# Performance work log

Measured on AMD Instinct MI355X. Metric: run time of the kernel, lower is better.

The kernel has to match this reference:

```python
import jax, jax.numpy as jnp
import numpy as np
from jax import lax

B, T, C = 4, 1024, 1024
H, HEAD = 16, 64            # n_head, head size (K == V == HEAD)
TM_DIM, TD_DIM = 32, 64     # TIME_MIX_EXTRA_DIM, W_MIX_EXTRA_DIM
N_LAYER, LAYER_ID = 24, 12
EPS = 1e-5
HEAD_DIV = 8.0              # head_size_divisor


def setup_inputs() -> dict:
    key = jax.random.key(0)
    ks = jax.random.split(key, 10)
    r1 = 1.0 - LAYER_ID / N_LAYER          # ratio_1_to_almost0
    r0 = LAYER_ID / max(N_LAYER - 1, 1)    # ratio_0_to_1
    ddd = np.arange(C, dtype=np.float64) / C
    x_maa = (1.0 - ddd ** r1).astype(np.float32)
    r_maa = (1.0 - ddd ** (0.5 * r1)).astype(np.float32)
    v_maa = (1.0 - (ddd ** r1 + 0.3 * r0)).astype(np.float32)
    n = np.arange(H * HEAD, dtype=np.float64)
    denom = max(H * HEAD - 1, 1)
    time_decay = (-6.0 + 5.0 * (n / denom) ** (0.7 + 1.3 * r0)).reshape(H, HEAD).astype(np.float32)
    zig = (((np.arange(H * HEAD) + 1) % 3) - 1) * 0.1
    time_first = (r0 * (1.0 - n / denom) + zig).reshape(H, HEAD).astype(np.float32)

    def unif(k, shape, s=0.01):
        return jax.random.uniform(k, shape, jnp.float32, -s, s)

    return {
        "x": jax.random.normal(ks[0], (B, T, C), jnp.float32),
        "x_maa": jnp.asarray(x_maa),
        "w_maa": jnp.asarray(x_maa),
        "k_maa": jnp.asarray(x_maa),
        "v_maa": jnp.asarray(v_maa),
        "r_maa": jnp.asarray(r_maa),
        "g_maa": jnp.asarray(r_maa),
        "tm_w1": unif(ks[1], (C, 5 * TM_DIM)),
        "tm_w2": unif(ks[2], (5, TM_DIM, C)),
        "td_w1": unif(ks[3], (C, TD_DIM)),
        "td_w2": unif(ks[4], (TD_DIM, C)),
        "time_decay": jnp.asarray(time_decay),
        "time_first": jnp.asarray(time_first),
        "Wr": jax.random.normal(ks[5], (C, H * HEAD), jnp.float32) * 0.02,
        "Wk": jax.random.normal(ks[6], (C, H * HEAD), jnp.float32) * 0.02,
        "Wv": jax.random.normal(ks[7], (C, H * HEAD), jnp.float32) * 0.02,
        "Wg": jax.random.normal(ks[8], (C, H * HEAD), jnp.float32) * 0.02,
        "Wo": jax.random.normal(ks[9], (H * HEAD, C), jnp.float32) * 0.02,
        "ln_w": jnp.ones((H * HEAD,), jnp.float32),
        "ln_b": jnp.zeros((H * HEAD,), jnp.float32),
    }


def reference(x, x_maa, w_maa, k_maa, v_maa, r_maa, g_maa,
              tm_w1, tm_w2, td_w1, td_w2, time_decay, time_first,
              Wr, Wk, Wv, Wg, Wo, ln_w, ln_b):
    B, T, C = x.shape
    H, K = time_decay.shape
    V = Wv.shape[1] // H
    # token shift: sx = x_{t-1} - x_t (zero-padded at t=0)
    sx = jnp.concatenate([jnp.zeros_like(x[:, :1]), x[:, :-1]], axis=1) - x
    # data-dependent token-mix LoRA: 5 mixing deltas
    mix = jnp.tanh((x + sx * x_maa) @ tm_w1).reshape(B, T, 5, TM_DIM)
    mix = jnp.einsum('btfd,fdc->fbtc', mix, tm_w2)  # [5,B,T,C]
    mw, mk, mv, mr, mg = mix
    wx = x + sx * (w_maa + mw)
    kx = x + sx * (k_maa + mk)
    vx = x + sx * (v_maa + mv)
    rx = x + sx * (r_maa + mr)
    gx = x + sx * (g_maa + mg)
    r = (rx @ Wr).reshape(B, T, H, K)
    k = (kx @ Wk).reshape(B, T, H, K)
    v = (vx @ Wv).reshape(B, T, H, V)
    g = jax.nn.silu(gx @ Wg)                         # [B,T,H*V]
    # data-dependent decay via LoRA, then double-exp squash into (0,1)
    w = time_decay[None, None] + (jnp.tanh(wx @ td_w1) @ td_w2).reshape(B, T, H, K)
    w = jnp.exp(-jnp.exp(w))                         # [B,T,H,K]
    u = time_first                                   # [H,K]

    def step(s, inp):
        rt, kt, vt, wt = inp                         # [B,H,K],[B,H,K],[B,H,V],[B,H,K]
        kv = kt[..., None] * vt[..., None, :]        # [B,H,K,V] outer product
        y = jnp.einsum('bhk,bhkv->bhv', rt, s + u[None, :, :, None] * kv)
        return wt[..., None] * s + kv, y

    s0 = jnp.zeros((B, H, K, V), x.dtype)
    xs = (jnp.moveaxis(r, 1, 0), jnp.moveaxis(k, 1, 0),
          jnp.moveaxis(v, 1, 0), jnp.moveaxis(w, 1, 0))
    _, ys = lax.scan(step, s0, xs)                   # ys: [T,B,H,V]
    out = jnp.moveaxis(ys, 0, 1).reshape(B, T, H, V) / HEAD_DIV
    # GroupNorm with n_kv_head groups over dim_v channels -> per-head norm
    mu = out.mean(-1, keepdims=True)
    var = out.var(-1, keepdims=True)
    out = ((out - mu) * lax.rsqrt(var + EPS)).reshape(B, T, H * V) * ln_w + ln_b
    return (out * g) @ Wo
```

## Files before the change

### kernel.cpp

```cpp
#include <hip/hip_runtime.h>
#include <hip/hip_bf16.h>
#include <math.h>
#include <stdint.h>

constexpr int Bn = 4, Tn = 1024, Cn = 1024, Hn = 16;
constexpr int BT = Bn * Tn;
constexpr long long BTC = (long long)BT * Cn;
constexpr int CL = 64;
constexpr int NC = Tn / CL;

typedef __bf16 bf16x8_t __attribute__((ext_vector_type(8)));
typedef float f32x4_t __attribute__((ext_vector_type(4)));
typedef unsigned short us8_t __attribute__((ext_vector_type(8)));

__device__ __forceinline__ unsigned short f2bf_bits(float v) {
    __hip_bfloat16 h = __float2bfloat16(v);
    return *reinterpret_cast<unsigned short*>(&h);
}
__device__ __forceinline__ float bfbits2f(unsigned short u) {
    unsigned int x = (unsigned int)u << 16;
    return __uint_as_float(x);
}

__device__ __forceinline__ void gload16(const void* g, void* l) {
    auto const* gp = reinterpret_cast<const unsigned int __attribute__((address_space(1)))*>(
        reinterpret_cast<uintptr_t>(g));
    auto* lp = reinterpret_cast<unsigned int __attribute__((address_space(3)))*>(
        reinterpret_cast<uintptr_t>(l));
    __builtin_amdgcn_global_load_lds(gp, lp, 16, 0, 0);
}

__global__ __launch_bounds__(256) void prep_mixin(const float* __restrict__ x,
                                                  const float* __restrict__ x_maa,
                                                  __hip_bfloat16* __restrict__ out) {
    long long q = (long long)blockIdx.x * 256 + threadIdx.x;
    if (q * 4 >= BTC) return;
    long long idx = q * 4;
    int c = (int)(idx & (Cn - 1));
    long long bt = idx >> 10;
    int t = (int)(bt & (Tn - 1));
    float4 xv = *reinterpret_cast<const float4*>(x + idx);
    float4 xp = (t > 0) ? *reinterpret_cast<const float4*>(x + idx - Cn)
                        : make_float4(0.f, 0.f, 0.f, 0.f);
    float4 ma = *reinterpret_cast<const float4*>(x_maa + c);
    ushort4 o;
    o.x = f2bf_bits(xv.x + (xp.x - xv.x) * ma.x);
    o.y = f2bf_bits(xv.y + (xp.y - xv.y) * ma.y);
    o.z = f2bf_bits(xv.z + (xp.z - xv.z) * ma.z);
    o.w = f2bf_bits(xv.w + (xp.w - xv.w) * ma.w);
    *reinterpret_cast<ushort4*>(out + idx) = o;
}

__global__ __launch_bounds__(256) void transp5(const float* __restrict__ W0,
                                               const float* __restrict__ W1,
                                               const float* __restrict__ W2,
                                               const float* __restrict__ W3,
                                               const float* __restrict__ W4,
                                               __hip_bfloat16* __restrict__ T0,
                                               __hip_bfloat16* __restrict__ T1,
                                               __hip_bfloat16* __restrict__ T2,
                                               __hip_bfloat16* __restrict__ T3,
                                               __hip_bfloat16* __restrict__ T4) {
    int z = blockIdx.z;
    const float* W = (z == 0) ? W0 : (z == 1) ? W1 : (z == 2) ? W2 : (z == 3) ? W3 : W4;
    __hip_bfloat16* Wt = (z == 0) ? T0 : (z == 1) ? T1 : (z == 2) ? T2 : (z == 3) ? T3 : T4;
    __shared__ float tile[32][33];
    int c0 = blockIdx.x * 32, r0 = blockIdx.y * 32;
    int tx = threadIdx.x & 31, ty = threadIdx.x >> 5;
    #pragma unroll
    for (int i = 0; i < 4; i++)
        tile[ty + 8 * i][tx] = W[(size_t)(r0 + ty + 8 * i) * Cn + c0 + tx];
    __syncthreads();
    #pragma unroll
    for (int i = 0; i < 4; i++)
        Wt[(size_t)(c0 + ty + 8 * i) * Cn + r0 + tx] = __float2bfloat16(tile[tx][ty + 8 * i]);
}

__global__ __launch_bounds__(256) void transp_bf16(const float* __restrict__ W,
                                                   __hip_bfloat16* __restrict__ Wt,
                                                   int R, int Cc) {
    __shared__ float tile[32][33];
    int c0 = blockIdx.x * 32, r0 = blockIdx.y * 32;
    int tx = threadIdx.x & 31, ty = threadIdx.x >> 5;
    #pragma unroll
    for (int i = 0; i < 4; i++)
        tile[ty + 8 * i][tx] = W[(size_t)(r0 + ty + 8 * i) * Cc + c0 + tx];
    __syncthreads();
    #pragma unroll
    for (int i = 0; i < 4; i++)
        Wt[(size_t)(c0 + ty + 8 * i) * R + r0 + tx] = __float2bfloat16(tile[tx][ty + 8 * i]);
}

template <int EPI>
__global__ __launch_bounds__(256) void gemm_f32(const float* __restrict__ A,
                                                const float* __restrict__ Bm,
                                                float* __restrict__ C,
                                                int M, int N, int K,
                                                const float* __restrict__ extra) {
    __shared__ float As[16][64];
    __shared__ float Bs[16][64];
    int tid = threadIdx.x;
    int m0 = blockIdx.y * 64, n0 = blockIdx.x * 64;
    int tx = tid & 15, ty = tid >> 4;
    int ar = tid >> 2, ac = (tid & 3) * 4;
    int br = tid >> 4, bc = (tid & 15) * 4;
    float acc[4][4] = {};

    for (int k0 = 0; k0 < K; k0 += 16) {
        const float* ap = A + (size_t)(m0 + ar) * K + k0 + ac;
        float4 av = *reinterpret_cast<const float4*>(ap);
        As[ac + 0][ar] = av.x; As[ac + 1][ar] = av.y;
        As[ac + 2][ar] = av.z; As[ac + 3][ar] = av.w;
        float4 bv = *reinterpret_cast<const float4*>(Bm + (size_t)(k0 + br) * N + n0 + bc);
        *reinterpret_cast<float4*>(&Bs[br][bc]) = bv;
        __syncthreads();
        #pragma unroll
        for (int kk = 0; kk < 16; kk++) {
            float4 a4 = *reinterpret_cast<const float4*>(&As[kk][ty * 4]);
            float4 b4 = *reinterpret_cast<const float4*>(&Bs[kk][tx * 4]);
            float aa[4] = {a4.x, a4.y, a4.z, a4.w};
            float bb[4] = {b4.x, b4.y, b4.z, b4.w};
            #pragma unroll
            for (int i = 0; i < 4; i++)
                #pragma unroll
                for (int j = 0; j < 4; j++)
                    acc[i][j] = fmaf(aa[i], bb[j], acc[i][j]);
        }
        __syncthreads();
    }

    #pragma unroll
    for (int i = 0; i < 4; i++) {
        int row = m0 + ty * 4 + i;
        #pragma unroll
        for (int j = 0; j < 4; j++) {
            int col = n0 + tx * 4 + j;
            float v = acc[i][j];
            if (EPI == 3) v = -expf(extra[col] + v);
            C[(size_t)row * N + col] = v;
        }
    }
}

template <int KS>
__global__ __launch_bounds__(256) void gemm_f32_splitk(const float* __restrict__ A,
                                                       const float* __restrict__ Bm,
                                                       float* __restrict__ part,
                                                       int M, int N, int K) {
    __shared__ float As[16][64];
    __shared__ float Bs[16][64];
    int tid = threadIdx.x;
    int kp = blockIdx.x;
    int m0 = blockIdx.y * 64;
    int kbeg = kp * (K / KS), kend = kbeg + K / KS;
    int tx = tid & 15, ty = tid >> 4;
    int ar = tid >> 2, ac = (tid & 3) * 4;
    int br = tid >> 4, bc = (tid & 15) * 4;
    float acc[4][4] = {};

    for (int k0 = kbeg; k0 < kend; k0 += 16) {
        float4 av = *reinterpret_cast<const float4*>(A + (size_t)(m0 + ar) * K + k0 + ac);
        As[ac + 0][ar] = av.x; As[ac + 1][ar] = av.y;
        As[ac + 2][ar] = av.z; As[ac + 3][ar] = av.w;
        *reinterpret_cast<float4*>(&Bs[br][bc]) =
            *reinterpret_cast<const float4*>(Bm + (size_t)(k0 + br) * N + bc);
        __syncthreads();
        #pragma unroll
        for (int kk = 0; kk < 16; kk++) {
            float4 a4 = *reinterpret_cast<const float4*>(&As[kk][ty * 4]);
            float4 b4 = *reinterpret_cast<const float4*>(&Bs[kk][tx * 4]);
            float aa[4] = {a4.x, a4.y, a4.z, a4.w};
            float bb[4] = {b4.x, b4.y, b4.z, b4.w};
            #pragma unroll
            for (int i = 0; i < 4; i++)
                #pragma unroll
                for (int j = 0; j < 4; j++)
                    acc[i][j] = fmaf(aa[i], bb[j], acc[i][j]);
        }
        __syncthreads();
    }
    #pragma unroll
    for (int i = 0; i < 4; i++) {
        int row = m0 + ty * 4 + i;
        #pragma unroll
        for (int j = 0; j < 4; j++)
            part[((size_t)kp * M + row) * N + tx * 4 + j] = acc[i][j];
    }
}

template <int KS>
__global__ __launch_bounds__(256) void splitk_reduce_tanh(const float* __restrict__ part,
                                                          float* __restrict__ outp,
                                                          int total, size_t stride) {
    int i = blockIdx.x * 256 + threadIdx.x;
    if (i >= total) return;
    float s = 0.f;
    #pragma unroll
    for (int kp = 0; kp < KS; kp++) s += part[kp * stride + i];
    outp[i] = tanhf(s);
}

template <int KS>
__global__ __launch_bounds__(256) void gemm_mfma_sk(const __hip_bfloat16* __restrict__ A,
                                                    const __hip_bfloat16* __restrict__ Bt,
                                                    float* __restrict__ part,
                                                    int M, int N, int K) {
    __shared__ alignas(16) unsigned short As[64 * 64];
    __shared__ alignas(16) unsigned short Bs[128 * 64];
    int tid = threadIdx.x;
    int m0 = blockIdx.y * 64, n0 = blockIdx.x * 128;
    int kp = blockIdx.z;
    int kbeg = kp * (K / KS), kend = kbeg + K / KS;
    int wave = tid >> 6, lane = tid & 63;
    int wm = (wave & 1) * 32, wn = (wave >> 1) * 64;
    int l15 = lane & 15, l4 = lane >> 4;
    f32x4_t acc[2][4] = {};

    for (int k0 = kbeg; k0 < kend; k0 += 64) {
        #pragma unroll
        for (int p = 0; p < 2; p++) {
            int cch = tid + p * 256;
            int row = cch >> 3, slot = cch & 7;
            int s2 = slot ^ (row & 7);
            *reinterpret_cast<us8_t*>(&As[row * 64 + s2 * 8]) =
                *reinterpret_cast<const us8_t*>(&A[(size_t)(m0 + row) * K + k0 + slot * 8]);
        }
        #pragma unroll
        for (int p = 0; p < 4; p++) {
            int cch = tid + p * 256;
            int row = cch >> 3, slot = cch & 7;
            int s2 = slot ^ (row & 7);
            int rowg = n0 + row; if (rowg > N - 1) rowg = N - 1;
            *reinterpret_cast<us8_t*>(&Bs[row * 64 + s2 * 8]) =
                *reinterpret_cast<const us8_t*>(&Bt[(size_t)rowg * K + k0 + slot * 8]);
        }
        __syncthreads();
        #pragma unroll
        for (int kw = 0; kw < 2; kw++) {
            int slot = kw * 4 + l4;
            bf16x8_t af[2], bfr[4];
            #pragma unroll
            for (int f = 0; f < 2; f++) {
                int ar = wm + f * 16 + l15;
                af[f] = *reinterpret_cast<const bf16x8_t*>(&As[ar * 64 + (slot ^ (ar & 7)) * 8]);
            }
            #pragma unroll
            for (int f = 0; f < 4; f++) {
                int br = wn + f * 16 + l15;
                bfr[f] = *reinterpret_cast<const bf16x8_t*>(&Bs[br * 64 + (slot ^ (br & 7)) * 8]);
            }
            #pragma unroll
            for (int i = 0; i < 2; i++)
                #pragma unroll
                for (int j = 0; j < 4; j++)
                    acc[i][j] = __builtin_amdgcn_mfma_f32_16x16x32_bf16(af[i], bfr[j], acc[i][j], 0, 0, 0);
        }
        __syncthreads();
    }

    #pragma unroll
    for (int i = 0; i < 2; i++) {
        int rbase = m0 + wm + i * 16 + l4 * 4;
        #pragma unroll
        for (int j = 0; j < 4; j++) {
            int col = n0 + wn + j * 16 + l15;
            if (col < N) {
                #pragma unroll
                for (int q = 0; q < 4; q++)
                    part[((size_t)kp * M + rbase + q) * N + col] = acc[i][j][q];
            }
        }
    }
}

__global__ __launch_bounds__(256) void gemm_qkvg(const __hip_bfloat16* __restrict__ A0,
                                                 const __hip_bfloat16* __restrict__ A1,
                                                 const __hip_bfloat16* __restrict__ A2,
                                                 const __hip_bfloat16* __restrict__ A3,
                                                 const __hip_bfloat16* __restrict__ B0,
                                                 const __hip_bfloat16* __restrict__ B1,
                                                 const __hip_bfloat16* __restrict__ B2,
                                                 const __hip_bfloat16* __restrict__ B3,
                                                 __hip_bfloat16* __restrict__ C0,
                                                 __hip_bfloat16* __restrict__ C1,
                                                 __hip_bfloat16* __restrict__ C2,
                                                 __hip_bfloat16* __restrict__ C3,
                                                 int M, int N, int K) {
    int g = blockIdx.z;
    const __hip_bfloat16* A  = (g == 0) ? A0 : (g == 1) ? A1 : (g == 2) ? A2 : A3;
    const __hip_bfloat16* Bt = (g == 0) ? B0 : (g == 1) ? B1 : (g == 2) ? B2 : B3;
    __hip_bfloat16* Co = (g == 0) ? C0 : (g == 1) ? C1 : (g == 2) ? C2 : C3;
    __shared__ alignas(16) unsigned short As[64 * 64];
    __shared__ alignas(16) unsigned short Bs[128 * 64];
    int tid = threadIdx.x;
    int m0 = blockIdx.x * 64, n0 = blockIdx.y * 128;
    int wave = tid >> 6, lane = tid & 63;
    int wm = (wave & 1) * 32, wn = (wave >> 1) * 64;
    int l15 = lane & 15, l4 = lane >> 4;
    int lrow = lane >> 3, ls2 = lane & 7;
    f32x4_t acc[2][4] = {};

    for (int k0 = 0; k0 < K; k0 += 64) {
        #pragma unroll
        for (int ci = 0; ci < 2; ci++) {
            int r0 = wave * 16 + ci * 8;
            int row = r0 + lrow;
            int gs = ls2 ^ (row & 7);
            gload16(&A[(size_t)(m0 + row) * K + k0 + gs * 8], &As[r0 * 64]);
        }
        #pragma unroll
        for (int ci = 0; ci < 4; ci++) {
            int r0 = wave * 32 + ci * 8;
            int row = r0 + lrow;
            int gs = ls2 ^ (row & 7);
            gload16(&Bt[(size_t)(n0 + row) * K + k0 + gs * 8], &Bs[r0 * 64]);
        }
        __syncthreads();
        #pragma unroll
        for (int kw = 0; kw < 2; kw++) {
            int slot = kw * 4 + l4;
            bf16x8_t af[2], bfr[4];
            #pragma unroll
            for (int f = 0; f < 2; f++) {
                int ar = wm + f * 16 + l15;
                af[f] = *reinterpret_cast<const bf16x8_t*>(&As[ar * 64 + (slot ^ (ar & 7)) * 8]);
            }
            #pragma unroll
            for (int f = 0; f < 4; f++) {
                int br = wn + f * 16 + l15;
                bfr[f] = *reinterpret_cast<const bf16x8_t*>(&Bs[br * 64 + (slot ^ (br & 7)) * 8]);
            }
            #pragma unroll
            for (int i = 0; i < 2; i++)
                #pragma unroll
                for (int j = 0; j < 4; j++)
                    acc[i][j] = __builtin_amdgcn_mfma_f32_16x16x32_bf16(af[i], bfr[j], acc[i][j], 0, 0, 0);
        }
        __syncthreads();
    }

    #pragma unroll
    for (int i = 0; i < 2; i++) {
        int rbase = m0 + wm + i * 16 + l4 * 4;
        #pragma unroll
        for (int j = 0; j < 4; j++) {
            int col = n0 + wn + j * 16 + l15;
            #pragma unroll
            for (int q = 0; q < 4; q++) {
                float v = acc[i][j][q];
                if (g == 3) v = v / (1.f + expf(-v));
                Co[(size_t)(rbase + q) * N + col] = __float2bfloat16(v);
            }
        }
    }
}

__global__ __launch_bounds__(256) void gemm_mfma_gl(const __hip_bfloat16* __restrict__ A,
                                                    const __hip_bfloat16* __restrict__ Bt,
                                                    float* __restrict__ Cout,
                                                    int M, int N, int K) {
    __shared__ alignas(16) unsigned short As[64 * 64];
    __shared__ alignas(16) unsigned short Bs[128 * 64];
    int tid = threadIdx.x;
    int m0 = blockIdx.x * 64, n0 = blockIdx.y * 128;
    int wave = tid >> 6, lane = tid & 63;
    int wm = (wave & 1) * 32, wn = (wave >> 1) * 64;
    int l15 = lane & 15, l4 = lane >> 4;
    int lrow = lane >> 3, ls2 = lane & 7;
    f32x4_t acc[2][4] = {};

    for (int k0 = 0; k0 < K; k0 += 64) {
        #pragma unroll
        for (int ci = 0; ci < 2; ci++) {
            int r0 = wave * 16 + ci * 8;
            int row = r0 + lrow;
            int gs = ls2 ^ (row & 7);
            gload16(&A[(size_t)(m0 + row) * K + k0 + gs * 8], &As[r0 * 64]);
        }
        #pragma unroll
        for (int ci = 0; ci < 4; ci++) {
            int r0 = wave * 32 + ci * 8;
            int row = r0 + lrow;
            int gs = ls2 ^ (row & 7);
            gload16(&Bt[(size_t)(n0 + row) * K + k0 + gs * 8], &Bs[r0 * 64]);
        }
        __syncthreads();
        #pragma unroll
        for (int kw = 0; kw < 2; kw++) {
            int slot = kw * 4 + l4;
            bf16x8_t af[2], bfr[4];
            #pragma unroll
            for (int f = 0; f < 2; f++) {
                int ar = wm + f * 16 + l15;
                af[f] = *reinterpret_cast<const bf16x8_t*>(&As[ar * 64 + (slot ^ (ar & 7)) * 8]);
            }
            #pragma unroll
            for (int f = 0; f < 4; f++) {
                int br = wn + f * 16 + l15;
                bfr[f] = *reinterpret_cast<const bf16x8_t*>(&Bs[br * 64 + (slot ^ (br & 7)) * 8]);
            }
            #pragma unroll
            for (int i = 0; i < 2; i++)
                #pragma unroll
                for (int j = 0; j < 4; j++)
                    acc[i][j] = __builtin_amdgcn_mfma_f32_16x16x32_bf16(af[i], bfr[j], acc[i][j], 0, 0, 0);
        }
        __syncthreads();
    }

    #pragma unroll
    for (int i = 0; i < 2; i++) {
        int rbase = m0 + wm + i * 16 + l4 * 4;
        #pragma unroll
        for (int j = 0; j < 4; j++) {
            int col = n0 + wn + j * 16 + l15;
            #pragma unroll
            for (int q = 0; q < 4; q++)
                Cout[(size_t)(rbase + q) * N + col] = acc[i][j][q];
        }
    }
}

__global__ __launch_bounds__(256) void deltas_mix(const float* __restrict__ x,
                                                  const float* __restrict__ mix160,
                                                  const float* __restrict__ w2,
                                                  const float* __restrict__ wmaa,
                                                  const float* __restrict__ kmaa,
                                                  const float* __restrict__ vmaa,
                                                  const float* __restrict__ rmaa,
                                                  const float* __restrict__ gmaa,
                                                  float* __restrict__ wx,
                                                  __hip_bfloat16* __restrict__ kxb,
                                                  __hip_bfloat16* __restrict__ vxb,
                                                  __hip_bfloat16* __restrict__ rxb,
                                                  __hip_bfloat16* __restrict__ gxb) {
    int tid = threadIdx.x;
    int c4 = tid * 4;
    int r0 = blockIdx.x * 4;
    const float* mrow = mix160 + (size_t)r0 * 160;
    float xv[4][4], sx[4][4];
    #pragma unroll
    for (int r = 0; r < 4; r++) {
        int row = r0 + r;
        int t = row & (Tn - 1);
        size_t idx = (size_t)row * Cn + c4;
        float4 xvv = *reinterpret_cast<const float4*>(x + idx);
        float4 xp = (t > 0) ? *reinterpret_cast<const float4*>(x + idx - Cn)
                            : make_float4(0.f, 0.f, 0.f, 0.f);
        xv[r][0] = xvv.x; xv[r][1] = xvv.y; xv[r][2] = xvv.z; xv[r][3] = xvv.w;
        sx[r][0] = xp.x - xvv.x; sx[r][1] = xp.y - xvv.y;
        sx[r][2] = xp.z - xvv.z; sx[r][3] = xp.w - xvv.w;
    }
    #pragma unroll
    for (int f = 0; f < 5; f++) {
        float acc[4][4] = {};
        for (int dd = 0; dd < 32; dd++) {
            float4 wv = *reinterpret_cast<const float4*>(w2 + (size_t)(f * 32 + dd) * Cn + c4);
            float wvv[4] = {wv.x, wv.y, wv.z, wv.w};
            #pragma unroll
            for (int r = 0; r < 4; r++) {
                float ms = mrow[r * 160 + f * 32 + dd];
                #pragma unroll
                for (int j = 0; j < 4; j++)
                    acc[r][j] = fmaf(ms, wvv[j], acc[r][j]);
            }
        }
        const float* maa = (f == 0) ? wmaa : (f == 1) ? kmaa : (f == 2) ? vmaa
                         : (f == 3) ? rmaa : gmaa;
        float4 mv4 = *reinterpret_cast<const float4*>(maa + c4);
        float mvv[4] = {mv4.x, mv4.y, mv4.z, mv4.w};
        #pragma unroll
        for (int r = 0; r < 4; r++) {
            size_t idx = (size_t)(r0 + r) * Cn + c4;
            float val[4];
            #pragma unroll
            for (int j = 0; j < 4; j++)
                val[j] = xv[r][j] + sx[r][j] * (mvv[j] + acc[r][j]);
            if (f == 0) {
                *reinterpret_cast<float4*>(wx + idx) =
                    make_float4(val[0], val[1], val[2], val[3]);
            } else {
                ushort4 o;
                o.x = f2bf_bits(val[0]); o.y = f2bf_bits(val[1]);
                o.z = f2bf_bits(val[2]); o.w = f2bf_bits(val[3]);
                __hip_bfloat16* dst = (f == 1) ? kxb : (f == 2) ? vxb : (f == 3) ? rxb : gxb;
                *reinterpret_cast<ushort4*>(dst + idx) = o;
            }
        }
    }
}

__global__ __launch_bounds__(256) void chunk_summary(const __hip_bfloat16* __restrict__ kb,
                                                     const __hip_bfloat16* __restrict__ vb,
                                                     const float* __restrict__ lw,
                                                     float* __restrict__ Bc,
                                                     float* __restrict__ Wtot) {
    int bid = blockIdx.x;
    int c = bid & 15, h = (bid >> 4) & 15, b = bid >> 8;
    size_t gbase = ((size_t)(b * Tn + c * CL) * Hn + h) * 64;
    int tid = threadIdx.x;
    __shared__ float linc[64][68];
    __shared__ float wtp[4][64];
    __shared__ alignas(16) __hip_bfloat16 kdT[64][72];
    __shared__ alignas(16) __hip_bfloat16 vsT[64][72];
    int wave = tid >> 6, lane = tid & 63;
    {
        float acc = 0.f;
        #pragma unroll
        for (int i = 0; i < 16; i++) {
            int t = wave * 16 + i;
            acc += lw[gbase + (size_t)t * 1024 + lane];
            linc[t][lane] = acc;
        }
        wtp[wave][lane] = acc;
    }
    __syncthreads();
    {
        float off = 0.f;
        for (int g = 0; g < wave; g++) off += wtp[g][lane];
        #pragma unroll
        for (int i = 0; i < 16; i++) linc[wave * 16 + i][lane] += off;
    }
    __syncthreads();
    int t4 = tid >> 2, c0 = (tid & 3) * 16;
    #pragma unroll
    for (int i = 0; i < 4; i++) {
        int ch = c0 + i * 4;
        size_t ga = gbase + (size_t)t4 * 1024 + ch;
        ushort4 ku = *reinterpret_cast<const ushort4*>(kb + ga);
        ushort4 vu = *reinterpret_cast<const ushort4*>(vb + ga);
        float kk[4] = {bfbits2f(ku.x), bfbits2f(ku.y), bfbits2f(ku.z), bfbits2f(ku.w)};
        float vv[4] = {bfbits2f(vu.x), bfbits2f(vu.y), bfbits2f(vu.z), bfbits2f(vu.w)};
        #pragma unroll
        for (int j = 0; j < 4; j++) {
            float li = linc[t4][ch + j];
            float lend = linc[63][ch + j];
            kdT[ch + j][t4] = __float2bfloat16(kk[j] * expf(lend - li));
            vsT[ch + j][t4] = __float2bfloat16(vv[j]);
        }
    }
    if (tid < 64) Wtot[(size_t)bid * 64 + tid] = expf(linc[63][tid]);
    __syncthreads();
    int l15 = lane & 15, l4q = lane >> 4;
    #pragma unroll
    for (int nt = 0; nt < 4; nt++) {
        f32x4_t acc = {};
        #pragma unroll
        for (int kt = 0; kt < 2; kt++) {
            bf16x8_t a = *reinterpret_cast<const bf16x8_t*>(&kdT[wave * 16 + l15][kt * 32 + l4q * 8]);
            bf16x8_t bb = *reinterpret_cast<const bf16x8_t*>(&vsT[nt * 16 + l15][kt * 32 + l4q * 8]);
            acc = __builtin_amdgcn_mfma_f32_16x16x32_bf16(a, bb, acc, 0, 0, 0);
        }
        #pragma unroll
        for (int q = 0; q < 4; q++) {
            int krow = wave * 16 + l4q * 4 + q;
            Bc[(size_t)bid * 4096 + (size_t)krow * 64 + nt * 16 + l15] = acc[q];
        }
    }
}

__global__ __launch_bounds__(256) void chunk_scan(const float* __restrict__ Bc,
                                                  const float* __restrict__ Wtot,
                                                  float* __restrict__ SbufT) {
    int bid = blockIdx.x;
    int bh = bid >> 2, vg = bid & 3;
    int kk = threadIdx.x >> 2;
    int v = vg * 16 + (threadIdx.x & 3) * 4;
    float4 S = make_float4(0.f, 0.f, 0.f, 0.f);
    for (int c = 0; c < NC; c++) {
        size_t base = (size_t)(bh * NC + c) * 4096;
        SbufT[base + (size_t)(v + 0) * 64 + kk] = S.x;
        SbufT[base + (size_t)(v + 1) * 64 + kk] = S.y;
        SbufT[base + (size_t)(v + 2) * 64 + kk] = S.z;
        SbufT[base + (size_t)(v + 3) * 64 + kk] = S.w;
        float wt = Wtot[(size_t)(bh * NC + c) * 64 + kk];
        float4 b4 = *reinterpret_cast<const float4*>(Bc + base + (size_t)kk * 64 + v);
        S.x = fmaf(wt, S.x, b4.x);
        S.y = fmaf(wt, S.y, b4.y);
        S.z = fmaf(wt, S.z, b4.z);
        S.w = fmaf(wt, S.w, b4.w);
    }
}

__global__ __launch_bounds__(256) void chunk_out(const __hip_bfloat16* __restrict__ rb,
                                                 const __hip_bfloat16* __restrict__ kb,
                                                 const __hip_bfloat16* __restrict__ vb,
                                                 const float* __restrict__ lw,
                                                 const float* __restrict__ SbufT,
                                                 const float* __restrict__ tf,
                                                 float* __restrict__ y) {
    int bid = blockIdx.x;
    int c = bid & 15, h = (bid >> 4) & 15, b = bid >> 8;
    size_t gbase = ((size_t)(b * Tn + c * CL) * Hn + h) * 64;
    int tid = threadIdx.x;
    __shared__ alignas(16) __hip_bfloat16 qs[64][72];
    __shared__ alignas(16) __hip_bfloat16 ks[64][72];
    __shared__ alignas(16) __hip_bfloat16 vsT[64][72];
    __shared__ alignas(16) __hip_bfloat16 scT[64][72];
    __shared__ alignas(16) float uni[64 * 68];
    __shared__ float wtp[4][64];
    __shared__ float diag[64];
    float (*linc)[68] = reinterpret_cast<float(*)[68]>(uni);
    __hip_bfloat16 (*asb)[72] = reinterpret_cast<__hip_bfloat16(*)[72]>(uni);
    int wave = tid >> 6, lane = tid & 63;
    {
        float acc = 0.f;
        #pragma unroll
        for (int i = 0; i < 16; i++) {
            int t = wave * 16 + i;
            acc += lw[gbase + (size_t)t * 1024 + lane];
            linc[t][lane] = acc;
        }
        wtp[wave][lane] = acc;
    }
    __syncthreads();
    {
        float off = 0.f;
        for (int g = 0; g < wave; g++) off += wtp[g][lane];
        #pragma unroll
        for (int i = 0; i < 16; i++) linc[wave * 16 + i][lane] += off;
    }
    __syncthreads();
    int t4 = tid >> 2, c0 = (tid & 3) * 16;
    float dpart = 0.f;
    #pragma unroll
    for (int i = 0; i < 4; i++) {
        int ch = c0 + i * 4;
        size_t ga = gbase + (size_t)t4 * 1024 + ch;
        ushort4 ru = *reinterpret_cast<const ushort4*>(rb + ga);
        ushort4 ku = *reinterpret_cast<const ushort4*>(kb + ga);
        ushort4 vu = *reinterpret_cast<const ushort4*>(vb + ga);
        float4 l4v = *reinterpret_cast<const float4*>(lw + ga);
        float4 u4 = *reinterpret_cast<const float4*>(tf + h * 64 + ch);
        float4 s4 = *reinterpret_cast<const float4*>(SbufT + (size_t)bid * 4096 + (size_t)t4 * 64 + ch);
        float rr[4] = {bfbits2f(ru.x), bfbits2f(ru.y), bfbits2f(ru.z), bfbits2f(ru.w)};
        float kkv[4] = {bfbits2f(ku.x), bfbits2f(ku.y), bfbits2f(ku.z), bfbits2f(ku.w)};
        float vv[4] = {bfbits2f(vu.x), bfbits2f(vu.y), bfbits2f(vu.z), bfbits2f(vu.w)};
        float lwv[4] = {l4v.x, l4v.y, l4v.z, l4v.w};
        float uu[4] = {u4.x, u4.y, u4.z, u4.w};
        float ss[4] = {s4.x, s4.y, s4.z, s4.w};
        #pragma unroll
        for (int j = 0; j < 4; j++) {
            float li = linc[t4][ch + j];
            qs[t4][ch + j] = __float2bfloat16(rr[j] * expf(li - lwv[j]));
            ks[t4][ch + j] = __float2bfloat16(kkv[j] * expf(-li));
            vsT[ch + j][t4] = __float2bfloat16(vv[j]);
            scT[t4][ch + j] = __float2bfloat16(ss[j]);
            dpart = fmaf(rr[j] * uu[j], kkv[j], dpart);
        }
    }
    dpart += __shfl_xor(dpart, 1);
    dpart += __shfl_xor(dpart, 2);
    if ((tid & 3) == 0) diag[t4] = dpart;
    __syncthreads();
    int l15 = lane & 15, l4q = lane >> 4;
    #pragma unroll
    for (int nt = 0; nt < 4; nt++) {
        f32x4_t acc = {};
        if (nt <= wave) {
            #pragma unroll
            for (int kt = 0; kt < 2; kt++) {
                bf16x8_t a = *reinterpret_cast<const bf16x8_t*>(&qs[wave * 16 + l15][kt * 32 + l4q * 8]);
                bf16x8_t bb = *reinterpret_cast<const bf16x8_t*>(&ks[nt * 16 + l15][kt * 32 + l4q * 8]);
                acc = __builtin_amdgcn_mfma_f32_16x16x32_bf16(a, bb, acc, 0, 0, 0);
            }
        }
        #pragma unroll
        for (int q = 0; q < 4; q++) {
            int t = wave * 16 + l4q * 4 + q;
            int tau = nt * 16 + l15;
            float v = (tau < t) ? acc[q] : (tau == t ? diag[t] : 0.f);
            asb[t][tau] = __float2bfloat16(v);
        }
    }
    __syncthreads();
    #pragma unroll
    for (int nt = 0; nt < 4; nt++) {
        f32x4_t acc = {};
        int kmax = (wave >> 1) + 1;
        for (int kt = 0; kt < kmax; kt++) {
            bf16x8_t a = *reinterpret_cast<const bf16x8_t*>(&asb[wave * 16 + l15][kt * 32 + l4q * 8]);
            bf16x8_t bb = *reinterpret_cast<const bf16x8_t*>(&vsT[nt * 16 + l15][kt * 32 + l4q * 8]);
            acc = __builtin_amdgcn_mfma_f32_16x16x32_bf16(a, bb, acc, 0, 0, 0);
        }
        #pragma unroll
        for (int kt = 0; kt < 2; kt++) {
            bf16x8_t a = *reinterpret_cast<const bf16x8_t*>(&qs[wave * 16 + l15][kt * 32 + l4q * 8]);
            bf16x8_t bb = *reinterpret_cast<const bf16x8_t*>(&scT[nt * 16 + l15][kt * 32 + l4q * 8]);
            acc = __builtin_amdgcn_mfma_f32_16x16x32_bf16(a, bb, acc, 0, 0, 0);
        }
        #pragma unroll
        for (int q = 0; q < 4; q++) {
            int t = wave * 16 + l4q * 4 + q;
            y[gbase + (size_t)t * 1024 + nt * 16 + l15] = acc[q];
        }
    }
}

__global__ __launch_bounds__(256) void gn_mul(const float* __restrict__ y,
                                              const __hip_bfloat16* __restrict__ g,
                                              const float* __restrict__ lnw,
                                              const float* __restrict__ lnb,
                                              __hip_bfloat16* __restrict__ fin) {
    int tid = threadIdx.x;
    int lane = tid & 63;
    int wv = tid >> 6;
    int grp = blockIdx.x * 4 + wv;
    int h = grp & 15;
    size_t idx = (size_t)grp * 64 + lane;
    float val = y[idx] * 0.125f;
    float sum = val, sq = val * val;
    #pragma unroll
    for (int off = 32; off > 0; off >>= 1) {
        sum += __shfl_xor(sum, off, 64);
        sq  += __shfl_xor(sq,  off, 64);
    }
    float mu = sum * (1.f / 64.f);
    float var = sq * (1.f / 64.f) - mu * mu;
    float rs = rsqrtf(var + 1e-5f);
    float o = (val - mu) * rs * lnw[h * 64 + lane] + lnb[h * 64 + lane];
    fin[idx] = __float2bfloat16(o * __bfloat162float(g[idx]));
}

extern "C" void kernel_launch(void* const* d_in, const int* in_sizes, int n_in,
                              void* d_out, int out_size, void* d_ws, size_t ws_size,
                              hipStream_t stream) {
    (void)in_sizes; (void)n_in; (void)out_size; (void)ws_size;
    const float* x      = (const float*)d_in[0];
    const float* x_maa  = (const float*)d_in[1];
    const float* w_maa  = (const float*)d_in[2];
    const float* k_maa  = (const float*)d_in[3];
    const float* v_maa  = (const float*)d_in[4];
    const float* r_maa  = (const float*)d_in[5];
    const float* g_maa  = (const float*)d_in[6];
    const float* tm_w1  = (const float*)d_in[7];
    const float* tm_w2  = (const float*)d_in[8];
    const float* td_w1  = (const float*)d_in[9];
    const float* td_w2  = (const float*)d_in[10];
    const float* t_dec  = (const float*)d_in[11];
    const float* t_first= (const float*)d_in[12];
    const float* Wr     = (const float*)d_in[13];
    const float* Wk     = (const float*)d_in[14];
    const float* Wv     = (const float*)d_in[15];
    const float* Wg     = (const float*)d_in[16];
    const float* Wo     = (const float*)d_in[17];
    const float* ln_w   = (const float*)d_in[18];
    const float* ln_b   = (const float*)d_in[19];
    float* out = (float*)d_out;

    char* ws = (char*)d_ws;
    size_t off = 0;
    auto alloc = [&](size_t bytes) -> void* {
        void* p = ws + off;
        off = (off + bytes + 255) & ~(size_t)255;
        return p;
    };
    __hip_bfloat16* mixin = (__hip_bfloat16*)alloc(BTC * 2);
    float* mix160 = (float*)alloc((size_t)BT * 160 * 4);
    float* wxr    = (float*)alloc(BTC * 4);
    __hip_bfloat16* kxb = (__hip_bfloat16*)alloc(BTC * 2);
    __hip_bfloat16* vxb = (__hip_bfloat16*)alloc(BTC * 2);
    __hip_bfloat16* rxb = (__hip_bfloat16*)alloc(BTC * 2);
    __hip_bfloat16* gxb = (__hip_bfloat16*)alloc(BTC * 2);
    __hip_bfloat16* kb  = (__hip_bfloat16*)alloc(BTC * 2);
    __hip_bfloat16* vb  = (__hip_bfloat16*)alloc(BTC * 2);
    __hip_bfloat16* gb  = (__hip_bfloat16*)alloc(BTC * 2);
    float* wl1 = (float*)alloc((size_t)BT * 64 * 4);
    float* lwb = (float*)alloc(BTC * 4);
    __hip_bfloat16* WrT = (__hip_bfloat16*)alloc((size_t)Cn * Cn * 2);
    __hip_bfloat16* WkT = (__hip_bfloat16*)alloc((size_t)Cn * Cn * 2);
    __hip_bfloat16* WvT = (__hip_bfloat16*)alloc((size_t)Cn * Cn * 2);
    __hip_bfloat16* WgT = (__hip_bfloat16*)alloc((size_t)Cn * Cn * 2);
    __hip_bfloat16* WoT = (__hip_bfloat16*)alloc((size_t)Cn * Cn * 2);
    __hip_bfloat16* tmw1T = (__hip_bfloat16*)alloc((size_t)160 * Cn * 2);
    float* skpart = (float*)alloc((size_t)8 * BT * 64 * 4);
    float* lorapart = (float*)alloc((size_t)4 * BT * 160 * 4);
    __hip_bfloat16* rb = mixin;
    float* BcB   = wxr;
    float* ybuf  = wxr;
    float* WtB   = wl1;
    float* SbufT = (float*)rxb;
    __hip_bfloat16* fin = kxb;

    dim3 blk(256);
    transp5<<<dim3(32, 32, 5), blk, 0, stream>>>(Wr, Wk, Wv, Wg, Wo,
                                                 WrT, WkT, WvT, WgT, WoT);
    transp_bf16<<<dim3(5, 32), blk, 0, stream>>>(tm_w1, tmw1T, Cn, 160);
    prep_mixin<<<dim3((unsigned)(BTC / 1024)), blk, 0, stream>>>(x, x_maa, mixin);
    gemm_mfma_sk<4><<<dim3(2, 64, 4), blk, 0, stream>>>(mixin, tmw1T, lorapart, BT, 160, Cn);
    splitk_reduce_tanh<4><<<dim3((BT * 160 + 255) / 256), blk, 0, stream>>>(
        lorapart, mix160, BT * 160, (size_t)BT * 160);
    deltas_mix<<<dim3(BT / 4), blk, 0, stream>>>(x, mix160, tm_w2,
                                                 w_maa, k_maa, v_maa, r_maa, g_maa,
                                                 wxr, kxb, vxb, rxb, gxb);
    gemm_qkvg<<<dim3(64, 8, 4), blk, 0, stream>>>(rxb, kxb, vxb, gxb,
                                                  WrT, WkT, WvT, WgT,
                                                  rb, kb, vb, gb, BT, Cn, Cn);
    gemm_f32_splitk<8><<<dim3(8, 64), blk, 0, stream>>>(wxr, td_w1, skpart, BT, 64, Cn);
    splitk_reduce_tanh<8><<<dim3(BT * 64 / 256), blk, 0, stream>>>(skpart, wl1, BT * 64,
                                                                   (size_t)BT * 64);
    gemm_f32<3><<<dim3(16, 64), blk, 0, stream>>>(wl1, td_w2, lwb, BT, Cn, 64, t_dec);
    chunk_summary<<<dim3(Bn * Hn * NC), blk, 0, stream>>>(kb, vb, lwb, BcB, WtB);
    chunk_scan<<<dim3(Bn * Hn * 4), blk, 0, stream>>>(BcB, WtB, SbufT);
    chunk_out<<<dim3(Bn * Hn * NC), blk, 0, stream>>>(rb, kb, vb, lwb, SbufT, t_first, ybuf);
    gn_mul<<<dim3(BT * Hn / 4), blk, 0, stream>>>(ybuf, gb, ln_w, ln_b, fin);
    gemm_mfma_gl<<<dim3(64, 8), blk, 0, stream>>>(fin, WoT, out, BT, Cn, Cn);
}
```

Measured before the change: 216.0 us.

## Replace scalar FP32 LoRA-delta mix with bf16 MFMA GEMM plus elementwise fuse kernel

Replaces the FP32 FMA-loop deltas_mix kernel with two kernels. The first is a bf16 MFMA GEMM (K=32 per mix factor) that writes five delta tensors in bf16. The second is an elementwise kernel that combines x, the shifted x, the maa vectors and the deltas into the mixed inputs. The tanh'd LoRA activations and tm_w2 are now stored in bf16, and the workspace is shared between lorapart, skpart and the deltas. This moves the small matmul onto tensor cores at the cost of an extra 5xBTC bf16 round trip through memory and reduced precision in the deltas.

```diff
diff --git a/kernel.cpp b/kernel.cpp
--- a/kernel.cpp
+++ b/kernel.cpp
@@ -201,6 +201,18 @@
 }
 
 template <int KS>
+__global__ __launch_bounds__(256) void splitk_reduce_tanh_bf(const float* __restrict__ part,
+                                                             __hip_bfloat16* __restrict__ outp,
+                                                             int total, size_t stride) {
+    int i = blockIdx.x * 256 + threadIdx.x;
+    if (i >= total) return;
+    float s = 0.f;
+    #pragma unroll
+    for (int kp = 0; kp < KS; kp++) s += part[kp * stride + i];
+    outp[i] = __float2bfloat16(tanhf(s));
+}
+
+template <int KS>
 __global__ __launch_bounds__(256) void gemm_mfma_sk(const __hip_bfloat16* __restrict__ A,
                                                     const __hip_bfloat16* __restrict__ Bt,
                                                     float* __restrict__ part,
@@ -269,6 +281,109 @@
                 for (int q = 0; q < 4; q++)
                     part[((size_t)kp * M + rbase + q) * N + col] = acc[i][j][q];
             }
+        }
+    }
+}
+
+__global__ __launch_bounds__(256) void dmix_gemm(const __hip_bfloat16* __restrict__ A,
+                                                 const __hip_bfloat16* __restrict__ W2T,
+                                                 __hip_bfloat16* __restrict__ D) {
+    __shared__ alignas(16) unsigned short As[64 * 32];
+    __shared__ alignas(16) unsigned short Bs[128 * 32];
+    int tid = threadIdx.x;
+    int m0 = blockIdx.x * 64, n0 = blockIdx.y * 128;
+    int f  = blockIdx.z;
+    int wave = tid >> 6, lane = tid & 63;
+    int wm = (wave & 1) * 32, wn = (wave >> 1) * 64;
+    int l15 = lane & 15, l4 = lane >> 4;
+    int lrow2 = lane >> 2, ls = lane & 3;
+    f32x4_t acc[2][4] = {};
+
+    {
+        int row = wave * 16 + lrow2;
+        int gs = ls ^ (row & 3);
+        gload16(&A[(size_t)(m0 + row) * 160 + f * 32 + gs * 8], &As[(wave * 16) * 32]);
+    }
+    #pragma unroll
+    for (int ci = 0; ci < 2; ci++) {
+        int r0 = wave * 32 + ci * 16;
+        int row = r0 + lrow2;
+        int gs = ls ^ (row & 3);
+        gload16(&W2T[(size_t)(n0 + row) * 160 + f * 32 + gs * 8], &Bs[r0 * 32]);
+    }
+    __syncthreads();
+    bf16x8_t af[2], bfr[4];
+    #pragma unroll
+    for (int i = 0; i < 2; i++) {
+        int ar = wm + i * 16 + l15;
+        af[i] = *reinterpret_cast<const bf16x8_t*>(&As[ar * 32 + ((l4 ^ (ar & 3)) * 8)]);
+    }
+    #pragma unroll
+    for (int j = 0; j < 4; j++) {
+        int br = wn + j * 16 + l15;
+        bfr[j] = *reinterpret_cast<const bf16x8_t*>(&Bs[br * 32 + ((l4 ^ (br & 3)) * 8)]);
+    }
+    #pragma unroll
+    for (int i = 0; i < 2; i++)
+        #pragma unroll
+        for (int j = 0; j < 4; j++)
+            acc[i][j] = __builtin_amdgcn_mfma_f32_16x16x32_bf16(af[i], bfr[j], acc[i][j], 0, 0, 0);
+
+    __hip_bfloat16* Df = D + (size_t)f * BTC;
+    #pragma unroll
+    for (int i = 0; i < 2; i++) {
+        int rbase = m0 + wm + i * 16 + l4 * 4;
+        #pragma unroll
+        for (int j = 0; j < 4; j++) {
+            int col = n0 + wn + j * 16 + l15;
+            #pragma unroll
+            for (int q = 0; q < 4; q++)
+                Df[(size_t)(rbase + q) * Cn + col] = __float2bfloat16(acc[i][j][q]);
+        }
+    }
+}
+
+__global__ __launch_bounds__(256) void dmix_fuse(const float* __restrict__ x,
+                                                 const __hip_bfloat16* __restrict__ D,
+                                                 const float* __restrict__ wmaa,
+                                                 const float* __restrict__ kmaa,
+                                                 const float* __restrict__ vmaa,
+                                                 const float* __restrict__ rmaa,
+                                                 const float* __restrict__ gmaa,
+                                                 float* __restrict__ wx,
+                                                 __hip_bfloat16* __restrict__ kxb,
+                                                 __hip_bfloat16* __restrict__ vxb,
+                                                 __hip_bfloat16* __restrict__ rxb,
+                                                 __hip_bfloat16* __restrict__ gxb) {
+    long long q = (long long)blockIdx.x * 256 + threadIdx.x;
+    if (q * 4 >= BTC) return;
+    long long idx = q * 4;
+    int c = (int)(idx & (Cn - 1));
+    int t = (int)((idx >> 10) & (Tn - 1));
+    float4 xv = *reinterpret_cast<const float4*>(x + idx);
+    float4 xp = (t > 0) ? *reinterpret_cast<const float4*>(x + idx - Cn)
+                        : make_float4(0.f, 0.f, 0.f, 0.f);
+    float sx[4] = {xp.x - xv.x, xp.y - xv.y, xp.z - xv.z, xp.w - xv.w};
+    float xvv[4] = {xv.x, xv.y, xv.z, xv.w};
+    #pragma unroll
+    for (int f = 0; f < 5; f++) {
+        const float* maa = (f == 0) ? wmaa : (f == 1) ? kmaa : (f == 2) ? vmaa
+                         : (f == 3) ? rmaa : gmaa;
+        float4 m4 = *reinterpret_cast<const float4*>(maa + c);
+        float mm[4] = {m4.x, m4.y, m4.z, m4.w};
+        ushort4 d4 = *reinterpret_cast<const ushort4*>(D + (size_t)f * BTC + idx);
+        float dd[4] = {bfbits2f(d4.x), bfbits2f(d4.y), bfbits2f(d4.z), bfbits2f(d4.w)};
+        float val[4];
+        #pragma unroll
+        for (int j = 0; j < 4; j++) val[j] = xvv[j] + sx[j] * (mm[j] + dd[j]);
+        if (f == 0) {
+            *reinterpret_cast<float4*>(wx + idx) = make_float4(val[0], val[1], val[2], val[3]);
+        } else {
+            ushort4 o;
+            o.x = f2bf_bits(val[0]); o.y = f2bf_bits(val[1]);
+            o.z = f2bf_bits(val[2]); o.w = f2bf_bits(val[3]);
+            __hip_bfloat16* dst = (f == 1) ? kxb : (f == 2) ? vxb : (f == 3) ? rxb : gxb;
+            *reinterpret_cast<ushort4*>(dst + idx) = o;
         }
     }
 }
@@ -421,75 +536,6 @@
     }
 }
 
-__global__ __launch_bounds__(256) void deltas_mix(const float* __restrict__ x,
-                                                  const float* __restrict__ mix160,
-                                                  const float* __restrict__ w2,
-                                                  const float* __restrict__ wmaa,
-                                                  const float* __restrict__ kmaa,
-                                                  const float* __restrict__ vmaa,
-                                                  const float* __restrict__ rmaa,
-                                                  const float* __restrict__ gmaa,
-                                                  float* __restrict__ wx,
-                                                  __hip_bfloat16* __restrict__ kxb,
-                                                  __hip_bfloat16* __restrict__ vxb,
-                                                  __hip_bfloat16* __restrict__ rxb,
-                                                  __hip_bfloat16* __restrict__ gxb) {
-    int tid = threadIdx.x;
-    int c4 = tid * 4;
-    int r0 = blockIdx.x * 4;
-    const float* mrow = mix160 + (size_t)r0 * 160;
-    float xv[4][4], sx[4][4];
-    #pragma unroll
-    for (int r = 0; r < 4; r++) {
-        int row = r0 + r;
-        int t = row & (Tn - 1);
-        size_t idx = (size_t)row * Cn + c4;
-        float4 xvv = *reinterpret_cast<const float4*>(x + idx);
-        float4 xp = (t > 0) ? *reinterpret_cast<const float4*>(x + idx - Cn)
-                            : make_float4(0.f, 0.f, 0.f, 0.f);
-        xv[r][0] = xvv.x; xv[r][1] = xvv.y; xv[r][2] = xvv.z; xv[r][3] = xvv.w;
-        sx[r][0] = xp.x - xvv.x; sx[r][1] = xp.y - xvv.y;
-        sx[r][2] = xp.z - xvv.z; sx[r][3] = xp.w - xvv.w;
-    }
-    #pragma unroll
-    for (int f = 0; f < 5; f++) {
-        float acc[4][4] = {};
-        for (int dd = 0; dd < 32; dd++) {
-            float4 wv = *reinterpret_cast<const float4*>(w2 + (size_t)(f * 32 + dd) * Cn + c4);
-            float wvv[4] = {wv.x, wv.y, wv.z, wv.w};
-            #pragma unroll
-            for (int r = 0; r < 4; r++) {
-                float ms = mrow[r * 160 + f * 32 + dd];
-                #pragma unroll
-                for (int j = 0; j < 4; j++)
-                    acc[r][j] = fmaf(ms, wvv[j], acc[r][j]);
-            }
-        }
-        const float* maa = (f == 0) ? wmaa : (f == 1) ? kmaa : (f == 2) ? vmaa
-                         : (f == 3) ? rmaa : gmaa;
-        float4 mv4 = *reinterpret_cast<const float4*>(maa + c4);
-        float mvv[4] = {mv4.x, mv4.y, mv4.z, mv4.w};
-        #pragma unroll
-        for (int r = 0; r < 4; r++) {
-            size_t idx = (size_t)(r0 + r) * Cn + c4;
-            float val[4];
-            #pragma unroll
-            for (int j = 0; j < 4; j++)
-                val[j] = xv[r][j] + sx[r][j] * (mvv[j] + acc[r][j]);
-            if (f == 0) {
-                *reinterpret_cast<float4*>(wx + idx) =
-                    make_float4(val[0], val[1], val[2], val[3]);
-            } else {
-                ushort4 o;
-                o.x = f2bf_bits(val[0]); o.y = f2bf_bits(val[1]);
-                o.z = f2bf_bits(val[2]); o.w = f2bf_bits(val[3]);
-                __hip_bfloat16* dst = (f == 1) ? kxb : (f == 2) ? vxb : (f == 3) ? rxb : gxb;
-                *reinterpret_cast<ushort4*>(dst + idx) = o;
-            }
-        }
-    }
-}
-
 __global__ __launch_bounds__(256) void chunk_summary(const __hip_bfloat16* __restrict__ kb,
                                                      const __hip_bfloat16* __restrict__ vb,
                                                      const float* __restrict__ lw,
@@ -756,7 +802,7 @@
         return p;
     };
     __hip_bfloat16* mixin = (__hip_bfloat16*)alloc(BTC * 2);
-    float* mix160 = (float*)alloc((size_t)BT * 160 * 4);
+    __hip_bfloat16* mix160b = (__hip_bfloat16*)alloc((size_t)BT * 160 * 2);
     float* wxr    = (float*)alloc(BTC * 4);
     __hip_bfloat16* kxb = (__hip_bfloat16*)alloc(BTC * 2);
     __hip_bfloat16* vxb = (__hip_bfloat16*)alloc(BTC * 2);
@@ -773,8 +819,11 @@
     __hip_bfloat16* WgT = (__hip_bfloat16*)alloc((size_t)Cn * Cn * 2);
     __hip_bfloat16* WoT = (__hip_bfloat16*)alloc((size_t)Cn * Cn * 2);
     __hip_bfloat16* tmw1T = (__hip_bfloat16*)alloc((size_t)160 * Cn * 2);
-    float* skpart = (float*)alloc((size_t)8 * BT * 64 * 4);
-    float* lorapart = (float*)alloc((size_t)4 * BT * 160 * 4);
+    __hip_bfloat16* w2T   = (__hip_bfloat16*)alloc((size_t)Cn * 160 * 2);
+    char* big = (char*)alloc((size_t)5 * BTC * 2);
+    float* lorapart = (float*)big;
+    __hip_bfloat16* d5 = (__hip_bfloat16*)big;
+    float* skpart = (float*)big;
     __hip_bfloat16* rb = mixin;
     float* BcB   = wxr;
     float* ybuf  = wxr;
@@ -786,13 +835,15 @@
     transp5<<<dim3(32, 32, 5), blk, 0, stream>>>(Wr, Wk, Wv, Wg, Wo,
                                                  WrT, WkT, WvT, WgT, WoT);
     transp_bf16<<<dim3(5, 32), blk, 0, stream>>>(tm_w1, tmw1T, Cn, 160);
+    transp_bf16<<<dim3(32, 5), blk, 0, stream>>>(tm_w2, w2T, 160, Cn);
     prep_mixin<<<dim3((unsigned)(BTC / 1024)), blk, 0, stream>>>(x, x_maa, mixin);
     gemm_mfma_sk<4><<<dim3(2, 64, 4), blk, 0, stream>>>(mixin, tmw1T, lorapart, BT, 160, Cn);
-    splitk_reduce_tanh<4><<<dim3((BT * 160 + 255) / 256), blk, 0, stream>>>(
-        lorapart, mix160, BT * 160, (size_t)BT * 160);
-    deltas_mix<<<dim3(BT / 4), blk, 0, stream>>>(x, mix160, tm_w2,
-                                                 w_maa, k_maa, v_maa, r_maa, g_maa,
-                                                 wxr, kxb, vxb, rxb, gxb);
+    splitk_reduce_tanh_bf<4><<<dim3((BT * 160 + 255) / 256), blk, 0, stream>>>(
+        lorapart, mix160b, BT * 160, (size_t)BT * 160);
+    dmix_gemm<<<dim3(64, 8, 5), blk, 0, stream>>>(mix160b, w2T, d5);
+    dmix_fuse<<<dim3((unsigned)(BTC / 1024)), blk, 0, stream>>>(x, d5,
+                                                                w_maa, k_maa, v_maa, r_maa, g_maa,
+                                                                wxr, kxb, vxb, rxb, gxb);
     gemm_qkvg<<<dim3(64, 8, 4), blk, 0, stream>>>(rxb, kxb, vxb, gxb,
                                                   WrT, WkT, WvT, WgT,
                                                   rb, kb, vb, gb, BT, Cn, Cn);
```

Measured after the change: 211.6 us. 1.02x faster.
